# Kernel tuning notes

Measured on AMD Instinct MI355X. Metric: run time of the kernel, lower is better.

Reference implementation:

```python
import jax, jax.numpy as jnp
import numpy as np

N, E, D_IN, D_OUT = 50000, 800000, 32, 64


def setup_inputs() -> dict:
    key = jax.random.key(0)
    k1, k2, k3 = jax.random.split(key, 3)
    x = jax.random.normal(k1, (N, D_IN), dtype=jnp.float32)
    edge_index = jax.random.randint(k2, (2, E), 0, N)
    W = jax.random.normal(k3, (D_IN, D_OUT), dtype=jnp.float32) / np.sqrt(D_IN).astype(np.float32)
    b = jnp.zeros((D_OUT,), dtype=jnp.float32)
    return {"x": x, "edge_index": edge_index, "W": W, "b": b}


def gcn_conv(x, edge_index, W, b):
    n = x.shape[0]
    loop = jnp.arange(n)
    src = jnp.concatenate([edge_index[0], loop])  # message sources (x_j)
    dst = jnp.concatenate([edge_index[1], loop])  # aggregation targets
    xw = x @ W  # [N, D_OUT]
    deg = jax.ops.segment_sum(jnp.ones(src.shape[0], dtype=xw.dtype), dst, num_segments=n)
    dinv = jnp.where(deg > 0, jax.lax.rsqrt(jnp.where(deg > 0, deg, 1.0)), 0.0)
    norm = dinv[src] * dinv[dst]  # [E+N]
    msg = xw[src] * norm[:, None]  # gather + scale
    out = jax.ops.segment_sum(msg, dst, num_segments=n)  # scatter-add aggregate
    return out + b


def reference(x, edge_index, W, b):
    h = jax.nn.relu(gcn_conv(x, edge_index, W, b))
    # InnerProductDecoder over given edges: sigmoid(<h_i, h_j>)
    logits = jnp.sum(h[edge_index[0]] * h[edge_index[1]], axis=-1)  # [E]
    adj_pred = jax.nn.sigmoid(logits) + 1e-15
    return (adj_pred, edge_index)
```

## Files before the change

### kernel.cpp

```cpp
#include <hip/hip_runtime.h>
#include <hip/hip_fp8.h>

#define D_IN 32
#define D_OUT 64
#define BCAP 1280
#define NBMAX 800

__device__ __forceinline__ unsigned char f2fp8(float f) {
    __hip_fp8_e4m3 v(f);
    return (unsigned char)v.__x;
}
__device__ __forceinline__ float fp82f(unsigned char u) {
    __hip_fp8_e4m3 v;
    v.__x = (__hip_fp8_storage_t)u;
    return (float)v;
}
__device__ __forceinline__ float dot4fp8(unsigned int ua, unsigned int ub) {
    float s = 0.f;
#pragma unroll
    for (int k = 0; k < 4; ++k) {
        __hip_fp8_e4m3 fa, fb;
        fa.__x = (__hip_fp8_storage_t)(unsigned char)(ua >> (8 * k));
        fb.__x = (__hip_fp8_storage_t)(unsigned char)(ub >> (8 * k));
        s += (float)fa * (float)fb;
    }
    return s;
}

__global__ void __launch_bounds__(256) k_bin2(const int* __restrict__ src,
                                              const int* __restrict__ dst,
                                              int* __restrict__ bincnt,
                                              int* __restrict__ binbuf,
                                              int E, int NB, int chunk) {
    __shared__ int hist[NBMAX];
    __shared__ int base_[NBMAX];
    int t = threadIdx.x;
    int s0 = blockIdx.x * chunk;
    int s1 = s0 + chunk; if (s1 > E) s1 = E;
    if (s0 >= E) return;
    for (int i = t; i < NB; i += 256) hist[i] = 0;
    __syncthreads();
    for (int k = s0 + t * 4; k < s1; k += 1024) {
        if (k + 3 < s1) {
            int4 d4 = *(const int4*)(dst + k);
            atomicAdd(&hist[d4.x >> 6], 1);
            atomicAdd(&hist[d4.y >> 6], 1);
            atomicAdd(&hist[d4.z >> 6], 1);
            atomicAdd(&hist[d4.w >> 6], 1);
        } else {
            for (int e = k; e < s1; ++e) atomicAdd(&hist[dst[e] >> 6], 1);
        }
    }
    __syncthreads();
    for (int i = t; i < NB; i += 256) {
        int hv = hist[i];
        base_[i] = hv ? atomicAdd(&bincnt[i], hv) : 0;
        hist[i] = 0;
    }
    __syncthreads();
    for (int k = s0 + t * 4; k < s1; k += 1024) {
        if (k + 3 < s1) {
            int4 sv = *(const int4*)(src + k);
            int4 dv = *(const int4*)(dst + k);
            int s4[4] = {sv.x, sv.y, sv.z, sv.w};
            int d4[4] = {dv.x, dv.y, dv.z, dv.w};
#pragma unroll
            for (int u = 0; u < 4; ++u) {
                int d = d4[u], bin = d >> 6;
                int slot = base_[bin] + atomicAdd(&hist[bin], 1);
                if (slot < BCAP)
                    binbuf[(size_t)bin * BCAP + slot] = (s4[u] << 6) | (d & 63);
            }
        } else {
            for (int e = k; e < s1; ++e) {
                int d = dst[e], bin = d >> 6;
                int slot = base_[bin] + atomicAdd(&hist[bin], 1);
                if (slot < BCAP)
                    binbuf[(size_t)bin * BCAP + slot] = (src[e] << 6) | (d & 63);
            }
        }
    }
}

__global__ void __launch_bounds__(256) k_build(const float* __restrict__ x,
                                               const float* __restrict__ W,
                                               const int* __restrict__ bincnt,
                                               int* __restrict__ binbuf,
                                               float* __restrict__ dinv,
                                               int* __restrict__ offs, int* __restrict__ ends,
                                               unsigned char* __restrict__ xws, int N) {
    __shared__ float Ws[D_IN * D_OUT];
    __shared__ float xs[64 * D_IN];
    __shared__ int ebuf[BCAP];
    __shared__ int lcnt[64], lofs[65], lcur[64];
    __shared__ float ds[64];
    int bin = blockIdx.x, t = threadIdx.x;
    int node0 = bin * 64;
    for (int i = t; i < D_IN * D_OUT; i += 256) Ws[i] = W[i];
    for (int i = t; i < 64 * (D_IN / 4); i += 256) {
        int r = i >> 3, q = i & 7;
        int node = node0 + r;
        float4 v = make_float4(0.f, 0.f, 0.f, 0.f);
        if (node < N) v = *(const float4*)(x + (size_t)node * D_IN + q * 4);
        *(float4*)(xs + r * D_IN + q * 4) = v;
    }
    if (t < 64) { lcnt[t] = 0; lcur[t] = 0; }
    __syncthreads();
    int ns = min(bincnt[bin], BCAP);
    int* bb = binbuf + (size_t)bin * BCAP;
    for (int k = t; k < ns; k += 256) {
        int p = bb[k];
        ebuf[k] = p;
        atomicAdd(&lcnt[p & 63], 1);
    }
    __syncthreads();
    if (t == 0) {
        int r = 0;
#pragma unroll
        for (int i = 0; i < 64; ++i) { lofs[i] = r; r += lcnt[i]; }
        lofs[64] = r;
    }
    __syncthreads();
    if (t < 64) {
        float d = rsqrtf((float)(lcnt[t] + 1));
        ds[t] = d;
        int node = node0 + t;
        if (node < N) {
            dinv[node] = d;
            offs[node] = bin * BCAP + lofs[t];
            ends[node] = bin * BCAP + lofs[t + 1];
        }
    }
    __syncthreads();
    for (int k = t; k < ns; k += 256) {
        int p = ebuf[k];
        int d = p & 63;
        int slot = atomicAdd(&lcur[d], 1);
        bb[lofs[d] + slot] = p >> 6;
    }
#pragma unroll
    for (int i = 0; i < 16; ++i) {
        int idx = i * 256 + t;
        int ln = idx >> 6, c = idx & 63;
        int node = node0 + ln;
        if (node < N) {
            float s = 0.f;
#pragma unroll
            for (int k = 0; k < D_IN; ++k) s += xs[ln * D_IN + k] * Ws[k * D_OUT + c];
            xws[(size_t)node * D_OUT + c] = f2fp8(s * ds[ln]);
        }
    }
}

__global__ void k_agg(const unsigned char* __restrict__ xws, const float* __restrict__ dinv,
                      const int* __restrict__ offs, const int* __restrict__ ends,
                      const int* __restrict__ srcs,
                      const float* __restrict__ b, unsigned char* __restrict__ h, int n) {
    int g = blockIdx.x * blockDim.x + threadIdx.x;
    int d = g >> 6, c = g & 63;
    if (d >= n) return;
    float dd = dinv[d];
    float a0 = fp82f(xws[(size_t)d * D_OUT + c]);
    float a1 = 0.f, a2 = 0.f, a3 = 0.f;
    int kend = ends[d];
    for (int k = offs[d]; k < kend; k += 8) {
        int s[8];
        float v[8];
#pragma unroll
        for (int u = 0; u < 8; ++u) {
            int t = k + u;
            s[u] = srcs[t < kend ? t : kend - 1];
        }
#pragma unroll
        for (int u = 0; u < 8; ++u) {
            float x = fp82f(xws[(size_t)s[u] * D_OUT + c]);
            v[u] = (k + u < kend) ? x : 0.f;
        }
        a0 += v[0]; a1 += v[1]; a2 += v[2]; a3 += v[3];
        a0 += v[4]; a1 += v[5]; a2 += v[6]; a3 += v[7];
    }
    float r = dd * ((a0 + a1) + (a2 + a3)) + b[c];
    h[(size_t)d * D_OUT + c] = f2fp8(r > 0.f ? r : 0.f);
}

__global__ void k_decode(const int* __restrict__ e0, const int* __restrict__ e1,
                         const unsigned char* __restrict__ h, float* __restrict__ out, int E) {
    int g = blockIdx.x * blockDim.x + threadIdx.x;
    int e = g >> 2, q = g & 3;
    if (e >= E) return;
    int i = e0[e], j = e1[e];
    uint4 a = *(const uint4*)(h + (size_t)i * D_OUT + q * 16);
    uint4 bb = *(const uint4*)(h + (size_t)j * D_OUT + q * 16);
    float p = dot4fp8(a.x, bb.x) + dot4fp8(a.y, bb.y)
            + dot4fp8(a.z, bb.z) + dot4fp8(a.w, bb.w);
    p += __shfl_xor(p, 1, 64);
    p += __shfl_xor(p, 2, 64);
    if (q == 0) {
        out[e] = 1.0f / (1.0f + expf(-p)) + 1e-15f;
        out[E + e] = (float)i;
        out[2 * E + e] = (float)j;
    }
}

extern "C" void kernel_launch(void* const* d_in, const int* in_sizes, int n_in,
                              void* d_out, int out_size, void* d_ws, size_t ws_size,
                              hipStream_t stream) {
    const float* x = (const float*)d_in[0];
    const int*   ei = (const int*)d_in[1];
    const float* W = (const float*)d_in[2];
    const float* b = (const float*)d_in[3];

    const int N = in_sizes[0] / D_IN;
    const int E = in_sizes[1] / 2;
    const size_t NF = (size_t)N * D_OUT;
    const int NB = (N + 63) >> 6;

    float* out = (float*)d_out;

    char* base = (char*)d_ws;
    unsigned char* xws    = (unsigned char*)base;
    unsigned char* h      = (unsigned char*)(base + NF);
    float*         dinv   = (float*)(base + NF * 2);
    int*           offs   = (int*)(base + NF * 2 + (size_t)N * 4);
    int*           ends   = offs + N;
    int*           bincnt = ends + N;
    int*           binbuf = bincnt + NB;

    const int* srcv = ei;
    const int* dstv = ei + E;

    const int B = 256;
    const int gNF = (int)((NF + B - 1) / B);
    const int gD  = (int)(((long long)E * 4 + B - 1) / B);
    const int NBLK = 128;
    const int chunk = ((E + NBLK - 1) / NBLK + 3) & ~3;

    hipMemsetAsync(bincnt, 0, (size_t)NB * 4, stream);
    k_bin2  <<<NBLK, B, 0, stream>>>(srcv, dstv, bincnt, binbuf, E, NB, chunk);
    k_build <<<NB,   B, 0, stream>>>(x, W, bincnt, binbuf, dinv, offs, ends, xws, N);
    k_agg   <<<gNF,  B, 0, stream>>>(xws, dinv, offs, ends, binbuf, b, h, N);
    k_decode<<<gD,   B, 0, stream>>>(srcv, dstv, h, out, E);
}
```

Before: 86.94 us.

## Replace global-atomic binning with per-block cells, decode one edge per thread

The binning kernel drops its histogram pass and its global atomics on bin counters. Each block now writes edges into private fixed-capacity cells per bin, so no memset is needed. The build kernel gathers those cells through a prefix over block counts and writes sorted sources to a separate array. The decode kernel now handles one edge per thread with four 16-byte loads per row instead of four lanes plus shuffles. There is a risk of silently dropping edges when a block's cell exceeds 32 entries, and the build gather is serialized per cell.

```diff
diff --git a/kernel.cpp b/kernel.cpp
--- a/kernel.cpp
+++ b/kernel.cpp
@@ -3,8 +3,10 @@
 
 #define D_IN 32
 #define D_OUT 64
-#define BCAP 1280
 #define NBMAX 800
+#define BIN_BLKS 128
+#define CAP 32
+#define EBCAP 1536
 
 __device__ __forceinline__ unsigned char f2fp8(float f) {
     __hip_fp8_e4m3 v(f);
@@ -27,38 +29,18 @@
     return s;
 }
 
-__global__ void __launch_bounds__(256) k_bin2(const int* __restrict__ src,
-                                              const int* __restrict__ dst,
-                                              int* __restrict__ bincnt,
-                                              int* __restrict__ binbuf,
-                                              int E, int NB, int chunk) {
-    __shared__ int hist[NBMAX];
-    __shared__ int base_[NBMAX];
-    int t = threadIdx.x;
-    int s0 = blockIdx.x * chunk;
+__global__ void __launch_bounds__(512) k_bin(const int* __restrict__ src,
+                                             const int* __restrict__ dst,
+                                             int* __restrict__ cellcnt,
+                                             int* __restrict__ cells,
+                                             int E, int NB, int chunk) {
+    __shared__ int cur[NBMAX];
+    int t = threadIdx.x, blk = blockIdx.x;
+    int s0 = blk * chunk;
     int s1 = s0 + chunk; if (s1 > E) s1 = E;
-    if (s0 >= E) return;
-    for (int i = t; i < NB; i += 256) hist[i] = 0;
-    __syncthreads();
-    for (int k = s0 + t * 4; k < s1; k += 1024) {
-        if (k + 3 < s1) {
-            int4 d4 = *(const int4*)(dst + k);
-            atomicAdd(&hist[d4.x >> 6], 1);
-            atomicAdd(&hist[d4.y >> 6], 1);
-            atomicAdd(&hist[d4.z >> 6], 1);
-            atomicAdd(&hist[d4.w >> 6], 1);
-        } else {
-            for (int e = k; e < s1; ++e) atomicAdd(&hist[dst[e] >> 6], 1);
-        }
-    }
-    __syncthreads();
-    for (int i = t; i < NB; i += 256) {
-        int hv = hist[i];
-        base_[i] = hv ? atomicAdd(&bincnt[i], hv) : 0;
-        hist[i] = 0;
-    }
-    __syncthreads();
-    for (int k = s0 + t * 4; k < s1; k += 1024) {
+    for (int i = t; i < NB; i += 512) cur[i] = 0;
+    __syncthreads();
+    for (int k = s0 + t * 4; k < s1; k += 2048) {
         if (k + 3 < s1) {
             int4 sv = *(const int4*)(src + k);
             int4 dv = *(const int4*)(dst + k);
@@ -67,31 +49,35 @@
 #pragma unroll
             for (int u = 0; u < 4; ++u) {
                 int d = d4[u], bin = d >> 6;
-                int slot = base_[bin] + atomicAdd(&hist[bin], 1);
-                if (slot < BCAP)
-                    binbuf[(size_t)bin * BCAP + slot] = (s4[u] << 6) | (d & 63);
+                int pos = atomicAdd(&cur[bin], 1);
+                if (pos < CAP)
+                    cells[((size_t)bin * BIN_BLKS + blk) * CAP + pos] = (s4[u] << 6) | (d & 63);
             }
         } else {
             for (int e = k; e < s1; ++e) {
                 int d = dst[e], bin = d >> 6;
-                int slot = base_[bin] + atomicAdd(&hist[bin], 1);
-                if (slot < BCAP)
-                    binbuf[(size_t)bin * BCAP + slot] = (src[e] << 6) | (d & 63);
+                int pos = atomicAdd(&cur[bin], 1);
+                if (pos < CAP)
+                    cells[((size_t)bin * BIN_BLKS + blk) * CAP + pos] = (src[e] << 6) | (d & 63);
             }
         }
     }
+    __syncthreads();
+    for (int i = t; i < NB; i += 512) cellcnt[(size_t)blk * NB + i] = min(cur[i], CAP);
 }
 
 __global__ void __launch_bounds__(256) k_build(const float* __restrict__ x,
                                                const float* __restrict__ W,
-                                               const int* __restrict__ bincnt,
-                                               int* __restrict__ binbuf,
+                                               const int* __restrict__ cellcnt,
+                                               const int* __restrict__ cells,
                                                float* __restrict__ dinv,
                                                int* __restrict__ offs, int* __restrict__ ends,
-                                               unsigned char* __restrict__ xws, int N) {
+                                               int* __restrict__ srcs,
+                                               unsigned char* __restrict__ xws, int N, int NB) {
     __shared__ float Ws[D_IN * D_OUT];
     __shared__ float xs[64 * D_IN];
-    __shared__ int ebuf[BCAP];
+    __shared__ int ebuf[EBCAP];
+    __shared__ int ccnt[BIN_BLKS], coff[BIN_BLKS + 1];
     __shared__ int lcnt[64], lofs[65], lcur[64];
     __shared__ float ds[64];
     int bin = blockIdx.x, t = threadIdx.x;
@@ -105,30 +91,44 @@
         *(float4*)(xs + r * D_IN + q * 4) = v;
     }
     if (t < 64) { lcnt[t] = 0; lcur[t] = 0; }
-    __syncthreads();
-    int ns = min(bincnt[bin], BCAP);
-    int* bb = binbuf + (size_t)bin * BCAP;
-    for (int k = t; k < ns; k += 256) {
-        int p = bb[k];
-        ebuf[k] = p;
-        atomicAdd(&lcnt[p & 63], 1);
-    }
+    if (t < BIN_BLKS) ccnt[t] = cellcnt[(size_t)t * NB + bin];
     __syncthreads();
     if (t == 0) {
         int r = 0;
 #pragma unroll
+        for (int i = 0; i < BIN_BLKS; ++i) { coff[i] = r; r += ccnt[i]; }
+        coff[BIN_BLKS] = r;
+    }
+    __syncthreads();
+    if (t < BIN_BLKS) {
+        const int* cp = cells + ((size_t)bin * BIN_BLKS + t) * CAP;
+        int o = coff[t], cn = ccnt[t];
+        for (int k = 0; k < cn; ++k) {
+            if (o + k < EBCAP) {
+                int p = cp[k];
+                ebuf[o + k] = p;
+                atomicAdd(&lcnt[p & 63], 1);
+            }
+        }
+    }
+    __syncthreads();
+    int ns = min(coff[BIN_BLKS], EBCAP);
+    if (t == 0) {
+        int r = 0;
+#pragma unroll
         for (int i = 0; i < 64; ++i) { lofs[i] = r; r += lcnt[i]; }
         lofs[64] = r;
     }
     __syncthreads();
+    int binbase = bin * EBCAP;
     if (t < 64) {
         float d = rsqrtf((float)(lcnt[t] + 1));
         ds[t] = d;
         int node = node0 + t;
         if (node < N) {
             dinv[node] = d;
-            offs[node] = bin * BCAP + lofs[t];
-            ends[node] = bin * BCAP + lofs[t + 1];
+            offs[node] = binbase + lofs[t];
+            ends[node] = binbase + lofs[t + 1];
         }
     }
     __syncthreads();
@@ -136,7 +136,7 @@
         int p = ebuf[k];
         int d = p & 63;
         int slot = atomicAdd(&lcur[d], 1);
-        bb[lofs[d] + slot] = p >> 6;
+        srcs[binbase + lofs[d] + slot] = p >> 6;
     }
 #pragma unroll
     for (int i = 0; i < 16; ++i) {
@@ -173,8 +173,8 @@
         }
 #pragma unroll
         for (int u = 0; u < 8; ++u) {
-            float x = fp82f(xws[(size_t)s[u] * D_OUT + c]);
-            v[u] = (k + u < kend) ? x : 0.f;
+            float xv = fp82f(xws[(size_t)s[u] * D_OUT + c]);
+            v[u] = (k + u < kend) ? xv : 0.f;
         }
         a0 += v[0]; a1 += v[1]; a2 += v[2]; a3 += v[3];
         a0 += v[4]; a1 += v[5]; a2 += v[6]; a3 += v[7];
@@ -185,21 +185,20 @@
 
 __global__ void k_decode(const int* __restrict__ e0, const int* __restrict__ e1,
                          const unsigned char* __restrict__ h, float* __restrict__ out, int E) {
-    int g = blockIdx.x * blockDim.x + threadIdx.x;
-    int e = g >> 2, q = g & 3;
+    int e = blockIdx.x * blockDim.x + threadIdx.x;
     if (e >= E) return;
     int i = e0[e], j = e1[e];
-    uint4 a = *(const uint4*)(h + (size_t)i * D_OUT + q * 16);
-    uint4 bb = *(const uint4*)(h + (size_t)j * D_OUT + q * 16);
-    float p = dot4fp8(a.x, bb.x) + dot4fp8(a.y, bb.y)
-            + dot4fp8(a.z, bb.z) + dot4fp8(a.w, bb.w);
-    p += __shfl_xor(p, 1, 64);
-    p += __shfl_xor(p, 2, 64);
-    if (q == 0) {
-        out[e] = 1.0f / (1.0f + expf(-p)) + 1e-15f;
-        out[E + e] = (float)i;
-        out[2 * E + e] = (float)j;
-    }
+    const uint4* hi = (const uint4*)(h + (size_t)i * D_OUT);
+    const uint4* hj = (const uint4*)(h + (size_t)j * D_OUT);
+    uint4 a0 = hi[0], a1 = hi[1], a2 = hi[2], a3 = hi[3];
+    uint4 b0 = hj[0], b1 = hj[1], b2 = hj[2], b3 = hj[3];
+    float p = dot4fp8(a0.x, b0.x) + dot4fp8(a0.y, b0.y) + dot4fp8(a0.z, b0.z) + dot4fp8(a0.w, b0.w)
+            + dot4fp8(a1.x, b1.x) + dot4fp8(a1.y, b1.y) + dot4fp8(a1.z, b1.z) + dot4fp8(a1.w, b1.w)
+            + dot4fp8(a2.x, b2.x) + dot4fp8(a2.y, b2.y) + dot4fp8(a2.z, b2.z) + dot4fp8(a2.w, b2.w)
+            + dot4fp8(a3.x, b3.x) + dot4fp8(a3.y, b3.y) + dot4fp8(a3.z, b3.z) + dot4fp8(a3.w, b3.w);
+    out[e] = 1.0f / (1.0f + expf(-p)) + 1e-15f;
+    out[E + e] = (float)i;
+    out[2 * E + e] = (float)j;
 }
 
 extern "C" void kernel_launch(void* const* d_in, const int* in_sizes, int n_in,
@@ -218,26 +217,25 @@
     float* out = (float*)d_out;
 
     char* base = (char*)d_ws;
-    unsigned char* xws    = (unsigned char*)base;
-    unsigned char* h      = (unsigned char*)(base + NF);
-    float*         dinv   = (float*)(base + NF * 2);
-    int*           offs   = (int*)(base + NF * 2 + (size_t)N * 4);
-    int*           ends   = offs + N;
-    int*           bincnt = ends + N;
-    int*           binbuf = bincnt + NB;
+    unsigned char* xws     = (unsigned char*)base;
+    unsigned char* h       = (unsigned char*)(base + NF);
+    float*         dinv    = (float*)(base + NF * 2);
+    int*           offs    = (int*)(base + NF * 2 + (size_t)N * 4);
+    int*           ends    = offs + N;
+    int*           cellcnt = ends + N;
+    int*           srcs    = cellcnt + (size_t)BIN_BLKS * NB;
+    int*           cells   = srcs + (size_t)NB * EBCAP;
 
     const int* srcv = ei;
     const int* dstv = ei + E;
 
     const int B = 256;
     const int gNF = (int)((NF + B - 1) / B);
-    const int gD  = (int)(((long long)E * 4 + B - 1) / B);
-    const int NBLK = 128;
-    const int chunk = ((E + NBLK - 1) / NBLK + 3) & ~3;
-
-    hipMemsetAsync(bincnt, 0, (size_t)NB * 4, stream);
-    k_bin2  <<<NBLK, B, 0, stream>>>(srcv, dstv, bincnt, binbuf, E, NB, chunk);
-    k_build <<<NB,   B, 0, stream>>>(x, W, bincnt, binbuf, dinv, offs, ends, xws, N);
-    k_agg   <<<gNF,  B, 0, stream>>>(xws, dinv, offs, ends, binbuf, b, h, N);
-    k_decode<<<gD,   B, 0, stream>>>(srcv, dstv, h, out, E);
-}
+    const int gD  = (E + B - 1) / B;
+    const int chunk = ((E + BIN_BLKS - 1) / BIN_BLKS + 7) & ~7;
+
+    k_bin   <<<BIN_BLKS, 512, 0, stream>>>(srcv, dstv, cellcnt, cells, E, NB, chunk);
+    k_build <<<NB,  B, 0, stream>>>(x, W, cellcnt, cells, dinv, offs, ends, srcs, xws, N, NB);
+    k_agg   <<<gNF, B, 0, stream>>>(xws, dinv, offs, ends, srcs, b, h, N);
+    k_decode<<<gD,  B, 0, stream>>>(srcv, dstv, h, out, E);
+}
```

Result: slower. 90.36 us (+3.9%).
